# Optimization experiments

Measured on AMD Instinct MI355X. Metric: run time of the kernel, lower is better.

The kernel has to match this reference:

```python
import jax, jax.numpy as jnp
import numpy as np

H, D, RPE_DIM, LAYERS = 8, 64, 64, 3
GAMMA = 0.999  # fixed decay (use_decay=True, requires_grad=False)
EPS = 1e-8

def simple_rmsnorm(x):
    # SimpleRMSNorm: x / (||x||_2 * d^{-1/2} + eps), no learned scale
    rms = jnp.sqrt(jnp.sum(x * x, axis=-1, keepdims=True)) * (x.shape[-1] ** -0.5)
    return x / (rms + EPS)

def rpe_transform(idx, pos_proj_w, pos_proj_b, layer_ws, layer_bs, out_w, out_b):
    # idx: (n, 1) -> (H, n, D)
    x = idx @ pos_proj_w + pos_proj_b            # (n, RPE_DIM)
    for i in range(LAYERS):                       # residual=False -> sequential
        x = jax.nn.relu(simple_rmsnorm(x)) @ layer_ws[i] + layer_bs[i]
    x = jax.nn.relu(simple_rmsnorm(x)) @ out_w + out_b   # (n, H*D)
    n = x.shape[0]
    return x.reshape(n, H, D).transpose(1, 0, 2)  # (H, n, D)

def setup_inputs() -> dict:
    key = jax.random.key(0)
    ks = jax.random.split(key, 6)
    b, n = 8, 4096
    s = RPE_DIM ** -0.5
    return {
        "x": jax.random.normal(ks[0], (b, H, n, D), jnp.float32),
        "pos_proj_w": jax.random.normal(ks[1], (1, RPE_DIM), jnp.float32),
        "pos_proj_b": jnp.zeros((RPE_DIM,), jnp.float32),
        "layer_ws": jax.random.normal(ks[2], (LAYERS, RPE_DIM, RPE_DIM), jnp.float32) * s,
        "layer_bs": jnp.zeros((LAYERS, RPE_DIM), jnp.float32),
        "out_w": jax.random.normal(ks[3], (RPE_DIM, H * D), jnp.float32) * s,
        "out_b": jnp.zeros((H * D,), jnp.float32),
    }

def reference(x, pos_proj_w, pos_proj_b, layer_ws, layer_bs, out_w, out_b):
    b, h, n, d = x.shape
    _rpe = lambda idx: rpe_transform(idx, pos_proj_w, pos_proj_b, layer_ws, layer_bs, out_w, out_b)
    # relative-position kernel values (par_type=1: raw integer offsets)
    zero = _rpe(jnp.zeros((1, 1), x.dtype))                       # (H, 1, D)
    pos_idx = jnp.arange(1, n, dtype=x.dtype).reshape(n - 1, 1)   # 1..n-1
    pos = _rpe(pos_idx)                                           # (H, n-1, D)
    neg = _rpe(-pos_idx[::-1])                                    # -(n-1)..-1
    # fixed exponential decay gamma^|offset|
    coef = jnp.arange(1, n, dtype=x.dtype).reshape(1, n - 1, 1)
    gamma = jnp.full((h, 1, d), GAMMA, x.dtype) ** coef           # (H, n-1, D)
    pos = gamma * pos
    neg = gamma[:, ::-1, :] * neg
    # act_type='none' -> identity activation on a
    a = jnp.concatenate([zero, pos, zero, neg], axis=1)           # (H, 2n, D)
    # circular conv of length 2n realizes the Toeplitz matvec
    y = jnp.fft.rfft(x, n=2 * n, axis=-2)                         # (b,H,n+1?,D) complex
    v = jnp.fft.rfft(a, n=2 * n, axis=-2)[None]                   # (1,H,.,D)
    out = jnp.fft.irfft(v * y, n=2 * n, axis=-2)[:, :, :n, :]
    return out
```

## Files before the change

kernel.cpp:

```cpp
#include <hip/hip_runtime.h>
#include <math.h>

#define NF 8192

__device__ __forceinline__ int phys(int e) { return e ^ (((e >> 4) & 7) << 1); }

__device__ __forceinline__ float2 cmul(float2 a, float2 b) {
    return make_float2(a.x*b.x - a.y*b.y, a.x*b.y + a.y*b.x);
}
__device__ __forceinline__ float2 cmulc(float2 a, float2 b) {
    return make_float2(a.x*b.x + a.y*b.y, a.y*b.x - a.x*b.y);
}
__device__ __forceinline__ float2 cadd(float2 a, float2 b){ return make_float2(a.x+b.x, a.y+b.y); }
__device__ __forceinline__ float2 csub(float2 a, float2 b){ return make_float2(a.x-b.x, a.y-b.y); }
__device__ __forceinline__ float2 mnegi(float2 a){ return make_float2(a.y, -a.x); }
__device__ __forceinline__ float2 mposi(float2 a){ return make_float2(-a.y, a.x); }
#define RSQ2 0.70710678118654752f
__device__ __forceinline__ float2 mw81 (float2 a){ return make_float2( RSQ2*(a.x+a.y),  RSQ2*(a.y-a.x)); }
__device__ __forceinline__ float2 mw83 (float2 a){ return make_float2( RSQ2*(a.y-a.x), -RSQ2*(a.x+a.y)); }
__device__ __forceinline__ float2 mw81c(float2 a){ return make_float2( RSQ2*(a.x-a.y),  RSQ2*(a.x+a.y)); }
__device__ __forceinline__ float2 mw83c(float2 a){ return make_float2(-RSQ2*(a.x+a.y),  RSQ2*(a.x-a.y)); }

#define C16_1 0.92387953251128674f
#define S16_1 0.38268343236508978f
#define C16_2 0.70710678118654752f

__device__ __forceinline__ void dif8_core(float2& v0, float2& v1, float2& v2, float2& v3,
                                          float2& v4, float2& v5, float2& v6, float2& v7) {
    float2 t;
    t = csub(v0, v4); v0 = cadd(v0, v4); v4 = t;
    t = csub(v1, v5); v1 = cadd(v1, v5); v5 = mw81(t);
    t = csub(v2, v6); v2 = cadd(v2, v6); v6 = mnegi(t);
    t = csub(v3, v7); v3 = cadd(v3, v7); v7 = mw83(t);
    t = csub(v0, v2); v0 = cadd(v0, v2); v2 = t;
    t = csub(v1, v3); v1 = cadd(v1, v3); v3 = mnegi(t);
    t = csub(v4, v6); v4 = cadd(v4, v6); v6 = t;
    t = csub(v5, v7); v5 = cadd(v5, v7); v7 = mnegi(t);
    t = csub(v0, v1); v0 = cadd(v0, v1); v1 = t;
    t = csub(v2, v3); v2 = cadd(v2, v3); v3 = t;
    t = csub(v4, v5); v4 = cadd(v4, v5); v5 = t;
    t = csub(v6, v7); v6 = cadd(v6, v7); v7 = t;
}

__device__ __forceinline__ void dit8_core(float2& v0, float2& v1, float2& v2, float2& v3,
                                          float2& v4, float2& v5, float2& v6, float2& v7) {
    float2 t;
    t = csub(v0, v1); v0 = cadd(v0, v1); v1 = t;
    t = csub(v2, v3); v2 = cadd(v2, v3); v3 = t;
    t = csub(v4, v5); v4 = cadd(v4, v5); v5 = t;
    t = csub(v6, v7); v6 = cadd(v6, v7); v7 = t;
    t = v2;        v2 = csub(v0, t); v0 = cadd(v0, t);
    t = mposi(v3); v3 = csub(v1, t); v1 = cadd(v1, t);
    t = v6;        v6 = csub(v4, t); v4 = cadd(v4, t);
    t = mposi(v7); v7 = csub(v5, t); v5 = cadd(v5, t);
    t = v4;        v4 = csub(v0, t); v0 = cadd(v0, t);
    t = mw81c(v5); v5 = csub(v1, t); v1 = cadd(v1, t);
    t = mposi(v6); v6 = csub(v2, t); v2 = cadd(v2, t);
    t = mw83c(v7); v7 = csub(v3, t); v3 = cadd(v3, t);
}

template<int M, int LM>
__device__ __forceinline__ void fwd8_lds(float2* Z, const float2* __restrict__ tw, int tid) {
    #pragma unroll
    for (int q = 0; q < 2; ++q) {
        int beta = tid + q*512;
        int i    = beta & (M-1);
        int base = ((beta >> LM) << (LM+3)) + i;
        float2 v0 = Z[phys(base        )];
        float2 v1 = Z[phys(base + 1*M)];
        float2 v2 = Z[phys(base + 2*M)];
        float2 v3 = Z[phys(base + 3*M)];
        float2 v4 = Z[phys(base + 4*M)];
        float2 v5 = Z[phys(base + 5*M)];
        float2 v6 = Z[phys(base + 6*M)];
        float2 v7 = Z[phys(base + 7*M)];
        dif8_core(v0,v1,v2,v3,v4,v5,v6,v7);
        int ts = (NF >> (LM+3)) * i;
        Z[phys(base        )] = v0;
        Z[phys(base + 4*M)] = cmul(v1, tw[ts*4]);
        Z[phys(base + 2*M)] = cmul(v2, tw[ts*2]);
        Z[phys(base + 6*M)] = cmul(v3, tw[ts*6]);
        Z[phys(base + 1*M)] = cmul(v4, tw[ts  ]);
        Z[phys(base + 5*M)] = cmul(v5, tw[ts*5]);
        Z[phys(base + 3*M)] = cmul(v6, tw[ts*3]);
        Z[phys(base + 7*M)] = cmul(v7, tw[ts*7]);
    }
}

template<int M, int LM>
__device__ __forceinline__ void inv8_lds(float2* Z, const float2* __restrict__ tw, int tid) {
    #pragma unroll
    for (int q = 0; q < 2; ++q) {
        int beta = tid + q*512;
        int i    = beta & (M-1);
        int base = ((beta >> LM) << (LM+3)) + i;
        int ts   = (NF >> (LM+3)) * i;
        float2 v0 = Z[phys(base        )];
        float2 v1 = cmulc(Z[phys(base + 4*M)], tw[ts*4]);
        float2 v2 = cmulc(Z[phys(base + 2*M)], tw[ts*2]);
        float2 v3 = cmulc(Z[phys(base + 6*M)], tw[ts*6]);
        float2 v4 = cmulc(Z[phys(base + 1*M)], tw[ts  ]);
        float2 v5 = cmulc(Z[phys(base + 5*M)], tw[ts*5]);
        float2 v6 = cmulc(Z[phys(base + 3*M)], tw[ts*3]);
        float2 v7 = cmulc(Z[phys(base + 7*M)], tw[ts*7]);
        dit8_core(v0,v1,v2,v3,v4,v5,v6,v7);
        Z[phys(base        )] = v0;
        Z[phys(base + 1*M)] = v1;
        Z[phys(base + 2*M)] = v2;
        Z[phys(base + 3*M)] = v3;
        Z[phys(base + 4*M)] = v4;
        Z[phys(base + 5*M)] = v5;
        Z[phys(base + 6*M)] = v6;
        Z[phys(base + 7*M)] = v7;
    }
}

__global__ void twiddle_kernel(float2* __restrict__ tw) {
    int j = blockIdx.x * 256 + threadIdx.x;
    double ang = -6.283185307179586476925286766559 * (double)j / 8192.0;
    tw[j] = make_float2((float)cos(ang), (float)sin(ang));
}

__global__ __launch_bounds__(256) void rpe_kernel(
    const float* __restrict__ pw,  const float* __restrict__ pb,
    const float* __restrict__ lws, const float* __restrict__ lbs,
    const float* __restrict__ ow,  const float* __restrict__ ob,
    float* __restrict__ a_buf)
{
    __shared__ float sW[3][64][64];
    __shared__ float sB[3][64];
    __shared__ float sPW[64], sPB[64];
    __shared__ float sAct[4][64];
    int tid = threadIdx.x;
    for (int idx = tid; idx < 3*64*64; idx += 256) ((float*)sW)[idx] = lws[idx];
    if (tid < 3*64) ((float*)sB)[tid] = lbs[tid];
    if (tid < 64) { sPW[tid] = pw[tid]; sPB[tid] = pb[tid]; }
    __syncthreads();

    int wave = tid >> 6, lane = tid & 63;
    int e = blockIdx.x * 4 + wave;
    float p = (e == 4096) ? 0.f : ((e < 4096) ? (float)e : (float)(e - 8192));
    int m = (e < 4096) ? e : (8192 - e);
    if (e == 4096) m = 0;
    float dec = exp2f(-0.0014434309482562475f * (float)m);

    float xv = fmaf(p, sPW[lane], sPB[lane]);
    for (int L = 0; L < 3; ++L) {
        float ss = xv * xv;
        #pragma unroll
        for (int o = 1; o < 64; o <<= 1) ss += __shfl_xor(ss, o);
        float act = fmaxf(xv / (sqrtf(ss) * 0.125f + 1e-8f), 0.f);
        sAct[wave][lane] = act;
        __syncthreads();
        float y0 = sB[L][lane], y1 = 0.f;
        #pragma unroll
        for (int k = 0; k < 64; k += 2) {
            y0 = fmaf(sAct[wave][k],   sW[L][k][lane],   y0);
            y1 = fmaf(sAct[wave][k+1], sW[L][k+1][lane], y1);
        }
        __syncthreads();
        xv = y0 + y1;
    }
    {
        float ss = xv * xv;
        #pragma unroll
        for (int o = 1; o < 64; o <<= 1) ss += __shfl_xor(ss, o);
        sAct[wave][lane] = fmaxf(xv / (sqrtf(ss) * 0.125f + 1e-8f), 0.f);
    }
    auto& sWo = sW[0];
    float res[8];
    for (int qq = 0; qq < 8; ++qq) {
        __syncthreads();
        for (int idx = tid; idx < 4096; idx += 256)
            ((float*)sWo)[idx] = ow[(size_t)(idx >> 6)*512 + qq*64 + (idx & 63)];
        __syncthreads();
        float y0 = ob[qq*64 + lane], y1 = 0.f, y2 = 0.f, y3 = 0.f;
        #pragma unroll
        for (int k = 0; k < 64; k += 4) {
            y0 = fmaf(sAct[wave][k],   sWo[k  ][lane], y0);
            y1 = fmaf(sAct[wave][k+1], sWo[k+1][lane], y1);
            y2 = fmaf(sAct[wave][k+2], sWo[k+2][lane], y2);
            y3 = fmaf(sAct[wave][k+3], sWo[k+3][lane], y3);
        }
        res[qq] = (y0+y1+y2+y3) * dec;
    }
    #pragma unroll
    for (int qq = 0; qq < 8; ++qq)
        a_buf[(size_t)(qq*64 + lane)*NF + e] = res[qq];
}

__global__ __launch_bounds__(512, 4) void afft_kernel(
    const float* __restrict__ a_buf, const float2* __restrict__ tw,
    float2* __restrict__ Afft)
{
    __shared__ __align__(16) float2 Z[NF];
    int cc = blockIdx.x, tid = threadIdx.x;
    const float* col = a_buf + (size_t)cc * NF;
    #pragma unroll
    for (int q = 0; q < 2; ++q) {
        int i = tid + q*512;
        float2 v0 = make_float2(col[i       ], 0.f);
        float2 v1 = make_float2(col[i + 1024], 0.f);
        float2 v2 = make_float2(col[i + 2048], 0.f);
        float2 v3 = make_float2(col[i + 3072], 0.f);
        float2 v4 = make_float2(col[i + 4096], 0.f);
        float2 v5 = make_float2(col[i + 5120], 0.f);
        float2 v6 = make_float2(col[i + 6144], 0.f);
        float2 v7 = make_float2(col[i + 7168], 0.f);
        dif8_core(v0,v1,v2,v3,v4,v5,v6,v7);
        int ts = i;
        Z[phys(i        )] = v0;
        Z[phys(i + 4096)] = cmul(v1, tw[ts*4]);
        Z[phys(i + 2048)] = cmul(v2, tw[ts*2]);
        Z[phys(i + 6144)] = cmul(v3, tw[ts*6]);
        Z[phys(i + 1024)] = cmul(v4, tw[ts  ]);
        Z[phys(i + 5120)] = cmul(v5, tw[ts*5]);
        Z[phys(i + 3072)] = cmul(v6, tw[ts*3]);
        Z[phys(i + 7168)] = cmul(v7, tw[ts*7]);
    }
    __syncthreads();
    fwd8_lds<128, 7>(Z, tw, tid);  __syncthreads();
    fwd8_lds<16,  4>(Z, tw, tid);  __syncthreads();
    {
        int c = tid, sw4 = c & 7;
        float4* Z4 = reinterpret_cast<float4*>(Z);
        float4* oc4 = reinterpret_cast<float4*>(Afft + (size_t)cc * NF);
        float2 z[16];
        #pragma unroll
        for (int j = 0; j < 8; ++j) {
            float4 wv = Z4[c*8 + (j ^ sw4)];
            z[2*j]   = make_float2(wv.x, wv.y);
            z[2*j+1] = make_float2(wv.z, wv.w);
        }
        dif8_core(z[0],z[2],z[4],z[6],z[8],z[10],z[12],z[14]);
        dif8_core(z[1],z[3],z[5],z[7],z[9],z[11],z[13],z[15]);
        #define A4K(k, ZE, ZO, WR, WI) { \
            float2 w = make_float2((WR)*(ZO).x - (WI)*(ZO).y, (WR)*(ZO).y + (WI)*(ZO).x); \
            float2 pp = cadd(ZE, w), rr = csub(ZE, w); \
            oc4[c*8 + (k)] = make_float4(pp.x, pp.y, rr.x, rr.y); }
        { float2 pp = cadd(z[0], z[1]), rr = csub(z[0], z[1]);
          oc4[c*8 + 0] = make_float4(pp.x, pp.y, rr.x, rr.y); }
        A4K(1, z[8],  z[9],   C16_1, -S16_1)
        A4K(2, z[4],  z[5],   C16_2, -C16_2)
        A4K(3, z[12], z[13],  S16_1, -C16_1)
        { float2 w = mnegi(z[3]);
          float2 pp = cadd(z[2], w), rr = csub(z[2], w);
          oc4[c*8 + 4] = make_float4(pp.x, pp.y, rr.x, rr.y); }
        A4K(5, z[10], z[11], -S16_1, -C16_1)
        A4K(6, z[6],  z[7],  -C16_2, -C16_2)
        A4K(7, z[14], z[15], -C16_1, -S16_1)
        #undef A4K
    }
}

__global__ __launch_bounds__(512, 4) void conv_kernel(
    const float* __restrict__ x, const float2* __restrict__ tw,
    const float2* __restrict__ Afft, float* __restrict__ out)
{
    __shared__ __align__(16) float2 Z[NF];
    int blk = blockIdx.x;
    int c8 = blk & 7, r = blk >> 3;
    int d  = ((c8 & 1) << 5) | (r & 31);
    int h  = (((r >> 5) & 3) << 1) | ((c8 >> 1) & 1);
    int bp = (((r >> 7) & 1) << 1) | ((c8 >> 2) & 1);
    int tid = threadIdx.x;
    size_t base0 = ((size_t)((bp*2 + 0)*8 + h) * 4096) * 64 + d;
    size_t base1 = ((size_t)((bp*2 + 1)*8 + h) * 4096) * 64 + d;

    #pragma unroll
    for (int q = 0; q < 2; ++q) {
        int i = tid + q*512;
        float2 v0 = make_float2(x[base0 + (size_t)(i       )*64], x[base1 + (size_t)(i       )*64]);
        float2 v1 = make_float2(x[base0 + (size_t)(i + 1024)*64], x[base1 + (size_t)(i + 1024)*64]);
        float2 v2 = make_float2(x[base0 + (size_t)(i + 2048)*64], x[base1 + (size_t)(i + 2048)*64]);
        float2 v3 = make_float2(x[base0 + (size_t)(i + 3072)*64], x[base1 + (size_t)(i + 3072)*64]);
        float2 v4 = v0;
        float2 v5 = mw81(v1);
        float2 v6 = mnegi(v2);
        float2 v7 = mw83(v3);
        float2 t;
        t = csub(v0, v2); v0 = cadd(v0, v2); v2 = t;
        t = csub(v1, v3); v1 = cadd(v1, v3); v3 = mnegi(t);
        t = csub(v4, v6); v4 = cadd(v4, v6); v6 = t;
        t = csub(v5, v7); v5 = cadd(v5, v7); v7 = mnegi(t);
        t = csub(v0, v1); v0 = cadd(v0, v1); v1 = t;
        t = csub(v2, v3); v2 = cadd(v2, v3); v3 = t;
        t = csub(v4, v5); v4 = cadd(v4, v5); v5 = t;
        t = csub(v6, v7); v6 = cadd(v6, v7); v7 = t;
        int ts = i;
        Z[phys(i        )] = v0;
        Z[phys(i + 4096)] = cmul(v1, tw[ts*4]);
        Z[phys(i + 2048)] = cmul(v2, tw[ts*2]);
        Z[phys(i + 6144)] = cmul(v3, tw[ts*6]);
        Z[phys(i + 1024)] = cmul(v4, tw[ts  ]);
        Z[phys(i + 5120)] = cmul(v5, tw[ts*5]);
        Z[phys(i + 3072)] = cmul(v6, tw[ts*3]);
        Z[phys(i + 7168)] = cmul(v7, tw[ts*7]);
    }
    __syncthreads();
    fwd8_lds<128, 7>(Z, tw, tid);  __syncthreads();
    fwd8_lds<16,  4>(Z, tw, tid);  __syncthreads();

    {
        int c = tid, sw4 = c & 7;
        float4* Z4 = reinterpret_cast<float4*>(Z);
        const float4* A4 = reinterpret_cast<const float4*>(Afft + (size_t)(h*64 + d)*NF);
        float2 z[16];
        #pragma unroll
        for (int j = 0; j < 8; ++j) {
            float4 wv = Z4[c*8 + (j ^ sw4)];
            z[2*j]   = make_float2(wv.x, wv.y);
            z[2*j+1] = make_float2(wv.z, wv.w);
        }
        dif8_core(z[0],z[2],z[4],z[6],z[8],z[10],z[12],z[14]);
        dif8_core(z[1],z[3],z[5],z[7],z[9],z[11],z[13],z[15]);
        #define P4K(k, ZE, ZO, WR, WI) { \
            float2 w = make_float2((WR)*(ZO).x - (WI)*(ZO).y, (WR)*(ZO).y + (WI)*(ZO).x); \
            float2 pp = cadd(ZE, w), rr = csub(ZE, w); \
            float4 av = A4[c*8 + (k)]; \
            pp = cmul(pp, make_float2(av.x, av.y)); \
            rr = cmul(rr, make_float2(av.z, av.w)); \
            ZE = cadd(pp, rr); \
            ZO = csub(pp, rr); }
        { float2 pp = cadd(z[0], z[1]), rr = csub(z[0], z[1]);
          float4 av = A4[c*8 + 0];
          pp = cmul(pp, make_float2(av.x, av.y));
          rr = cmul(rr, make_float2(av.z, av.w));
          z[0] = cadd(pp, rr); z[1] = csub(pp, rr); }
        P4K(1, z[8],  z[9],   C16_1, -S16_1)
        P4K(2, z[4],  z[5],   C16_2, -C16_2)
        P4K(3, z[12], z[13],  S16_1, -C16_1)
        { float2 w = mnegi(z[3]);
          float2 pp = cadd(z[2], w), rr = csub(z[2], w);
          float4 av = A4[c*8 + 4];
          pp = cmul(pp, make_float2(av.x, av.y));
          rr = cmul(rr, make_float2(av.z, av.w));
          z[2] = cadd(pp, rr); z[3] = csub(pp, rr); }
        P4K(5, z[10], z[11], -S16_1, -C16_1)
        P4K(6, z[6],  z[7],  -C16_2, -C16_2)
        P4K(7, z[14], z[15], -C16_1, -S16_1)
        #undef P4K
        z[3]  = mposi(z[3]);
        z[5]  = cmul(z[5],  make_float2( C16_2,  C16_2));
        z[7]  = cmul(z[7],  make_float2(-C16_2,  C16_2));
        z[9]  = cmul(z[9],  make_float2( C16_1,  S16_1));
        z[11] = cmul(z[11], make_float2(-S16_1,  C16_1));
        z[13] = cmul(z[13], make_float2( S16_1,  C16_1));
        z[15] = cmul(z[15], make_float2(-C16_1,  S16_1));
        dit8_core(z[0],z[2],z[4],z[6],z[8],z[10],z[12],z[14]);
        dit8_core(z[1],z[3],z[5],z[7],z[9],z[11],z[13],z[15]);
        #pragma unroll
        for (int j = 0; j < 8; ++j)
            Z4[c*8 + (j ^ sw4)] = make_float4(z[2*j].x, z[2*j].y, z[2*j+1].x, z[2*j+1].y);
    }
    __syncthreads();
    inv8_lds<16,  4>(Z, tw, tid);  __syncthreads();
    inv8_lds<128, 7>(Z, tw, tid);  __syncthreads();

    const float sc = 1.0f/8192.0f;
    #pragma unroll
    for (int q = 0; q < 2; ++q) {
        int i = tid + q*512;
        int ts = i;
        float2 v0 = Z[phys(i        )];
        float2 v1 = cmulc(Z[phys(i + 4096)], tw[ts*4]);
        float2 v2 = cmulc(Z[phys(i + 2048)], tw[ts*2]);
        float2 v3 = cmulc(Z[phys(i + 6144)], tw[ts*6]);
        float2 v4 = cmulc(Z[phys(i + 1024)], tw[ts  ]);
        float2 v5 = cmulc(Z[phys(i + 5120)], tw[ts*5]);
        float2 v6 = cmulc(Z[phys(i + 3072)], tw[ts*3]);
        float2 v7 = cmulc(Z[phys(i + 7168)], tw[ts*7]);
        float2 t;
        t = csub(v0, v1); v0 = cadd(v0, v1); v1 = t;
        t = csub(v2, v3); v2 = cadd(v2, v3); v3 = t;
        t = csub(v4, v5); v4 = cadd(v4, v5); v5 = t;
        t = csub(v6, v7); v6 = cadd(v6, v7); v7 = t;
        t = v2;        v2 = csub(v0, t); v0 = cadd(v0, t);
        t = mposi(v3); v3 = csub(v1, t); v1 = cadd(v1, t);
        t = v6;        v6 = csub(v4, t); v4 = cadd(v4, t);
        t = mposi(v7); v7 = csub(v5, t); v5 = cadd(v5, t);
        v0 = cadd(v0, v4);
        v1 = cadd(v1, mw81c(v5));
        v2 = cadd(v2, mposi(v6));
        v3 = cadd(v3, mw83c(v7));
        out[base0 + (size_t)(i       )*64] = v0.x * sc;
        out[base1 + (size_t)(i       )*64] = v0.y * sc;
        out[base0 + (size_t)(i + 1024)*64] = v1.x * sc;
        out[base1 + (size_t)(i + 1024)*64] = v1.y * sc;
        out[base0 + (size_t)(i + 2048)*64] = v2.x * sc;
        out[base1 + (size_t)(i + 2048)*64] = v2.y * sc;
        out[base0 + (size_t)(i + 3072)*64] = v3.x * sc;
        out[base1 + (size_t)(i + 3072)*64] = v3.y * sc;
    }
}

extern "C" void kernel_launch(void* const* d_in, const int* in_sizes, int n_in,
                              void* d_out, int out_size, void* d_ws, size_t ws_size,
                              hipStream_t stream) {
    const float* x   = (const float*)d_in[0];
    const float* pw  = (const float*)d_in[1];
    const float* pb  = (const float*)d_in[2];
    const float* lws = (const float*)d_in[3];
    const float* lbs = (const float*)d_in[4];
    const float* ow  = (const float*)d_in[5];
    const float* ob  = (const float*)d_in[6];
    float* out = (float*)d_out;
    char* ws = (char*)d_ws;
    float2* tw    = (float2*)ws;
    float*  a_buf = (float*)(ws + 65536);
    float2* Afft  = (float2*)(ws + 65536 + (size_t)512*NF*4);

    twiddle_kernel<<<32, 256, 0, stream>>>(tw);
    rpe_kernel<<<2048, 256, 0, stream>>>(pw, pb, lws, lbs, ow, ob, a_buf);
    afft_kernel<<<512, 512, 0, stream>>>(a_buf, tw, Afft);
    conv_kernel<<<2048, 512, 0, stream>>>(x, tw, Afft, out);
}
```

Baseline: 586.5 us.

## Compute FFT twiddles on the fly, batch RPE MLP, and coalesce spectrum layout

Removes the twiddle table kernel and instead computes twiddles in registers from a hardware sin/cos of the base angle plus complex powers, avoiding global twiddle loads. The RPE MLP kernel now processes 4 positions per wave with 512 threads, cutting syncs and reusing the staged output weights across positions. The Afft layout is transposed to [k][c], so adjacent threads read adjacent float4 entries in the conv kernel. Risks include lower twiddle accuracy from native sin/cos and from chained power multiplication, and extra ALU work in the FFT stages.

```diff
diff --git a/kernel.cpp b/kernel.cpp
--- a/kernel.cpp
+++ b/kernel.cpp
@@ -24,6 +24,11 @@
 #define C16_1 0.92387953251128674f
 #define S16_1 0.38268343236508978f
 #define C16_2 0.70710678118654752f
+
+__device__ __forceinline__ float2 twbase(int ts) {
+    float fa = (float)ts * (1.0f/8192.0f);
+    return make_float2(__builtin_amdgcn_cosf(fa), -__builtin_amdgcn_sinf(fa));
+}
 
 __device__ __forceinline__ void dif8_core(float2& v0, float2& v1, float2& v2, float2& v3,
                                           float2& v4, float2& v5, float2& v6, float2& v7) {
@@ -59,8 +64,17 @@
     t = mw83c(v7); v7 = csub(v3, t); v3 = cadd(v3, t);
 }
 
+#define TW_POWERS(ts) \
+    float2 w1 = twbase(ts); \
+    float2 w2 = cmul(w1, w1); \
+    float2 w3 = cmul(w2, w1); \
+    float2 w4 = cmul(w2, w2); \
+    float2 w5 = cmul(w3, w2); \
+    float2 w6 = cmul(w3, w3); \
+    float2 w7 = cmul(w4, w3);
+
 template<int M, int LM>
-__device__ __forceinline__ void fwd8_lds(float2* Z, const float2* __restrict__ tw, int tid) {
+__device__ __forceinline__ void fwd8_lds(float2* Z, int tid) {
     #pragma unroll
     for (int q = 0; q < 2; ++q) {
         int beta = tid + q*512;
@@ -75,34 +89,34 @@
         float2 v6 = Z[phys(base + 6*M)];
         float2 v7 = Z[phys(base + 7*M)];
         dif8_core(v0,v1,v2,v3,v4,v5,v6,v7);
-        int ts = (NF >> (LM+3)) * i;
+        TW_POWERS((NF >> (LM+3)) * i)
         Z[phys(base        )] = v0;
-        Z[phys(base + 4*M)] = cmul(v1, tw[ts*4]);
-        Z[phys(base + 2*M)] = cmul(v2, tw[ts*2]);
-        Z[phys(base + 6*M)] = cmul(v3, tw[ts*6]);
-        Z[phys(base + 1*M)] = cmul(v4, tw[ts  ]);
-        Z[phys(base + 5*M)] = cmul(v5, tw[ts*5]);
-        Z[phys(base + 3*M)] = cmul(v6, tw[ts*3]);
-        Z[phys(base + 7*M)] = cmul(v7, tw[ts*7]);
+        Z[phys(base + 4*M)] = cmul(v1, w4);
+        Z[phys(base + 2*M)] = cmul(v2, w2);
+        Z[phys(base + 6*M)] = cmul(v3, w6);
+        Z[phys(base + 1*M)] = cmul(v4, w1);
+        Z[phys(base + 5*M)] = cmul(v5, w5);
+        Z[phys(base + 3*M)] = cmul(v6, w3);
+        Z[phys(base + 7*M)] = cmul(v7, w7);
     }
 }
 
 template<int M, int LM>
-__device__ __forceinline__ void inv8_lds(float2* Z, const float2* __restrict__ tw, int tid) {
+__device__ __forceinline__ void inv8_lds(float2* Z, int tid) {
     #pragma unroll
     for (int q = 0; q < 2; ++q) {
         int beta = tid + q*512;
         int i    = beta & (M-1);
         int base = ((beta >> LM) << (LM+3)) + i;
-        int ts   = (NF >> (LM+3)) * i;
+        TW_POWERS((NF >> (LM+3)) * i)
         float2 v0 = Z[phys(base        )];
-        float2 v1 = cmulc(Z[phys(base + 4*M)], tw[ts*4]);
-        float2 v2 = cmulc(Z[phys(base + 2*M)], tw[ts*2]);
-        float2 v3 = cmulc(Z[phys(base + 6*M)], tw[ts*6]);
-        float2 v4 = cmulc(Z[phys(base + 1*M)], tw[ts  ]);
-        float2 v5 = cmulc(Z[phys(base + 5*M)], tw[ts*5]);
-        float2 v6 = cmulc(Z[phys(base + 3*M)], tw[ts*3]);
-        float2 v7 = cmulc(Z[phys(base + 7*M)], tw[ts*7]);
+        float2 v1 = cmulc(Z[phys(base + 4*M)], w4);
+        float2 v2 = cmulc(Z[phys(base + 2*M)], w2);
+        float2 v3 = cmulc(Z[phys(base + 6*M)], w6);
+        float2 v4 = cmulc(Z[phys(base + 1*M)], w1);
+        float2 v5 = cmulc(Z[phys(base + 5*M)], w5);
+        float2 v6 = cmulc(Z[phys(base + 3*M)], w3);
+        float2 v7 = cmulc(Z[phys(base + 7*M)], w7);
         dit8_core(v0,v1,v2,v3,v4,v5,v6,v7);
         Z[phys(base        )] = v0;
         Z[phys(base + 1*M)] = v1;
@@ -115,83 +129,83 @@
     }
 }
 
-__global__ void twiddle_kernel(float2* __restrict__ tw) {
-    int j = blockIdx.x * 256 + threadIdx.x;
-    double ang = -6.283185307179586476925286766559 * (double)j / 8192.0;
-    tw[j] = make_float2((float)cos(ang), (float)sin(ang));
-}
-
-__global__ __launch_bounds__(256) void rpe_kernel(
+
+__global__ __launch_bounds__(512) void rpe_kernel(
     const float* __restrict__ pw,  const float* __restrict__ pb,
     const float* __restrict__ lws, const float* __restrict__ lbs,
     const float* __restrict__ ow,  const float* __restrict__ ob,
     float* __restrict__ a_buf)
 {
     __shared__ float sW[3][64][64];
+    __shared__ float sWo[64][64];
     __shared__ float sB[3][64];
     __shared__ float sPW[64], sPB[64];
-    __shared__ float sAct[4][64];
+    __shared__ float sAct[8][4][64];
     int tid = threadIdx.x;
-    for (int idx = tid; idx < 3*64*64; idx += 256) ((float*)sW)[idx] = lws[idx];
-    if (tid < 3*64) ((float*)sB)[tid] = lbs[tid];
+    for (int idx = tid; idx < 3*64*64; idx += 512) ((float*)sW)[idx] = lws[idx];
+    if (tid < 192) ((float*)sB)[tid] = lbs[tid];
     if (tid < 64) { sPW[tid] = pw[tid]; sPB[tid] = pb[tid]; }
     __syncthreads();
 
-    int wave = tid >> 6, lane = tid & 63;
-    int e = blockIdx.x * 4 + wave;
-    float p = (e == 4096) ? 0.f : ((e < 4096) ? (float)e : (float)(e - 8192));
-    int m = (e < 4096) ? e : (8192 - e);
-    if (e == 4096) m = 0;
-    float dec = exp2f(-0.0014434309482562475f * (float)m);
-
-    float xv = fmaf(p, sPW[lane], sPB[lane]);
-    for (int L = 0; L < 3; ++L) {
+    int wv = tid >> 6, lane = tid & 63;
+    int e0 = blockIdx.x * 32 + wv * 4;
+    float dec[4];
+    #pragma unroll
+    for (int s = 0; s < 4; ++s) {
+        int e = e0 + s;
+        float p = (e == 4096) ? 0.f : ((e < 4096) ? (float)e : (float)(e - 8192));
+        int m = (e < 4096) ? e : (8192 - e);
+        if (e == 4096) m = 0;
+        dec[s] = exp2f(-0.0014434309482562475f * (float)m);
+
+        float xv = fmaf(p, sPW[lane], sPB[lane]);
+        #pragma unroll
+        for (int L = 0; L < 3; ++L) {
+            float ss = xv * xv;
+            #pragma unroll
+            for (int o = 1; o < 64; o <<= 1) ss += __shfl_xor(ss, o);
+            sAct[wv][s][lane] = fmaxf(xv / (sqrtf(ss) * 0.125f + 1e-8f), 0.f);
+            float y = sB[L][lane];
+            const float4* av = reinterpret_cast<const float4*>(sAct[wv][s]);
+            #pragma unroll
+            for (int k = 0; k < 16; ++k) {
+                float4 a4 = av[k];
+                y = fmaf(a4.x, sW[L][4*k  ][lane], y);
+                y = fmaf(a4.y, sW[L][4*k+1][lane], y);
+                y = fmaf(a4.z, sW[L][4*k+2][lane], y);
+                y = fmaf(a4.w, sW[L][4*k+3][lane], y);
+            }
+            xv = y;
+        }
         float ss = xv * xv;
         #pragma unroll
         for (int o = 1; o < 64; o <<= 1) ss += __shfl_xor(ss, o);
-        float act = fmaxf(xv / (sqrtf(ss) * 0.125f + 1e-8f), 0.f);
-        sAct[wave][lane] = act;
-        __syncthreads();
-        float y0 = sB[L][lane], y1 = 0.f;
-        #pragma unroll
-        for (int k = 0; k < 64; k += 2) {
-            y0 = fmaf(sAct[wave][k],   sW[L][k][lane],   y0);
-            y1 = fmaf(sAct[wave][k+1], sW[L][k+1][lane], y1);
-        }
-        __syncthreads();
-        xv = y0 + y1;
-    }
-    {
-        float ss = xv * xv;
-        #pragma unroll
-        for (int o = 1; o < 64; o <<= 1) ss += __shfl_xor(ss, o);
-        sAct[wave][lane] = fmaxf(xv / (sqrtf(ss) * 0.125f + 1e-8f), 0.f);
-    }
-    auto& sWo = sW[0];
-    float res[8];
+        sAct[wv][s][lane] = fmaxf(xv / (sqrtf(ss) * 0.125f + 1e-8f), 0.f);
+    }
     for (int qq = 0; qq < 8; ++qq) {
         __syncthreads();
-        for (int idx = tid; idx < 4096; idx += 256)
+        for (int idx = tid; idx < 4096; idx += 512)
             ((float*)sWo)[idx] = ow[(size_t)(idx >> 6)*512 + qq*64 + (idx & 63)];
         __syncthreads();
-        float y0 = ob[qq*64 + lane], y1 = 0.f, y2 = 0.f, y3 = 0.f;
-        #pragma unroll
-        for (int k = 0; k < 64; k += 4) {
-            y0 = fmaf(sAct[wave][k],   sWo[k  ][lane], y0);
-            y1 = fmaf(sAct[wave][k+1], sWo[k+1][lane], y1);
-            y2 = fmaf(sAct[wave][k+2], sWo[k+2][lane], y2);
-            y3 = fmaf(sAct[wave][k+3], sWo[k+3][lane], y3);
+        #pragma unroll
+        for (int s = 0; s < 4; ++s) {
+            float y = ob[qq*64 + lane];
+            const float4* av = reinterpret_cast<const float4*>(sAct[wv][s]);
+            #pragma unroll
+            for (int k = 0; k < 16; ++k) {
+                float4 a4 = av[k];
+                y = fmaf(a4.x, sWo[4*k  ][lane], y);
+                y = fmaf(a4.y, sWo[4*k+1][lane], y);
+                y = fmaf(a4.z, sWo[4*k+2][lane], y);
+                y = fmaf(a4.w, sWo[4*k+3][lane], y);
+            }
+            a_buf[(size_t)(qq*64 + lane)*NF + (e0 + s)] = y * dec[s];
         }
-        res[qq] = (y0+y1+y2+y3) * dec;
-    }
-    #pragma unroll
-    for (int qq = 0; qq < 8; ++qq)
-        a_buf[(size_t)(qq*64 + lane)*NF + e] = res[qq];
+    }
 }
 
 __global__ __launch_bounds__(512, 4) void afft_kernel(
-    const float* __restrict__ a_buf, const float2* __restrict__ tw,
-    float2* __restrict__ Afft)
+    const float* __restrict__ a_buf, float2* __restrict__ Afft)
 {
     __shared__ __align__(16) float2 Z[NF];
     int cc = blockIdx.x, tid = threadIdx.x;
@@ -208,19 +222,19 @@
         float2 v6 = make_float2(col[i + 6144], 0.f);
         float2 v7 = make_float2(col[i + 7168], 0.f);
         dif8_core(v0,v1,v2,v3,v4,v5,v6,v7);
-        int ts = i;
+        TW_POWERS(i)
         Z[phys(i        )] = v0;
-        Z[phys(i + 4096)] = cmul(v1, tw[ts*4]);
-        Z[phys(i + 2048)] = cmul(v2, tw[ts*2]);
-        Z[phys(i + 6144)] = cmul(v3, tw[ts*6]);
-        Z[phys(i + 1024)] = cmul(v4, tw[ts  ]);
-        Z[phys(i + 5120)] = cmul(v5, tw[ts*5]);
-        Z[phys(i + 3072)] = cmul(v6, tw[ts*3]);
-        Z[phys(i + 7168)] = cmul(v7, tw[ts*7]);
+        Z[phys(i + 4096)] = cmul(v1, w4);
+        Z[phys(i + 2048)] = cmul(v2, w2);
+        Z[phys(i + 6144)] = cmul(v3, w6);
+        Z[phys(i + 1024)] = cmul(v4, w1);
+        Z[phys(i + 5120)] = cmul(v5, w5);
+        Z[phys(i + 3072)] = cmul(v6, w3);
+        Z[phys(i + 7168)] = cmul(v7, w7);
     }
     __syncthreads();
-    fwd8_lds<128, 7>(Z, tw, tid);  __syncthreads();
-    fwd8_lds<16,  4>(Z, tw, tid);  __syncthreads();
+    fwd8_lds<128, 7>(Z, tid);  __syncthreads();
+    fwd8_lds<16,  4>(Z, tid);  __syncthreads();
     {
         int c = tid, sw4 = c & 7;
         float4* Z4 = reinterpret_cast<float4*>(Z);
@@ -237,15 +251,15 @@
         #define A4K(k, ZE, ZO, WR, WI) { \
             float2 w = make_float2((WR)*(ZO).x - (WI)*(ZO).y, (WR)*(ZO).y + (WI)*(ZO).x); \
             float2 pp = cadd(ZE, w), rr = csub(ZE, w); \
-            oc4[c*8 + (k)] = make_float4(pp.x, pp.y, rr.x, rr.y); }
+            oc4[(k)*512 + c] = make_float4(pp.x, pp.y, rr.x, rr.y); }
         { float2 pp = cadd(z[0], z[1]), rr = csub(z[0], z[1]);
-          oc4[c*8 + 0] = make_float4(pp.x, pp.y, rr.x, rr.y); }
+          oc4[0*512 + c] = make_float4(pp.x, pp.y, rr.x, rr.y); }
         A4K(1, z[8],  z[9],   C16_1, -S16_1)
         A4K(2, z[4],  z[5],   C16_2, -C16_2)
         A4K(3, z[12], z[13],  S16_1, -C16_1)
         { float2 w = mnegi(z[3]);
           float2 pp = cadd(z[2], w), rr = csub(z[2], w);
-          oc4[c*8 + 4] = make_float4(pp.x, pp.y, rr.x, rr.y); }
+          oc4[4*512 + c] = make_float4(pp.x, pp.y, rr.x, rr.y); }
         A4K(5, z[10], z[11], -S16_1, -C16_1)
         A4K(6, z[6],  z[7],  -C16_2, -C16_2)
         A4K(7, z[14], z[15], -C16_1, -S16_1)
@@ -254,8 +268,8 @@
 }
 
 __global__ __launch_bounds__(512, 4) void conv_kernel(
-    const float* __restrict__ x, const float2* __restrict__ tw,
-    const float2* __restrict__ Afft, float* __restrict__ out)
+    const float* __restrict__ x, const float2* __restrict__ Afft,
+    float* __restrict__ out)
 {
     __shared__ __align__(16) float2 Z[NF];
     int blk = blockIdx.x;
@@ -287,19 +301,19 @@
         t = csub(v2, v3); v2 = cadd(v2, v3); v3 = t;
         t = csub(v4, v5); v4 = cadd(v4, v5); v5 = t;
         t = csub(v6, v7); v6 = cadd(v6, v7); v7 = t;
-        int ts = i;
+        TW_POWERS(i)
         Z[phys(i        )] = v0;
-        Z[phys(i + 4096)] = cmul(v1, tw[ts*4]);
-        Z[phys(i + 2048)] = cmul(v2, tw[ts*2]);
-        Z[phys(i + 6144)] = cmul(v3, tw[ts*6]);
-        Z[phys(i + 1024)] = cmul(v4, tw[ts  ]);
-        Z[phys(i + 5120)] = cmul(v5, tw[ts*5]);
-        Z[phys(i + 3072)] = cmul(v6, tw[ts*3]);
-        Z[phys(i + 7168)] = cmul(v7, tw[ts*7]);
+        Z[phys(i + 4096)] = cmul(v1, w4);
+        Z[phys(i + 2048)] = cmul(v2, w2);
+        Z[phys(i + 6144)] = cmul(v3, w6);
+        Z[phys(i + 1024)] = cmul(v4, w1);
+        Z[phys(i + 5120)] = cmul(v5, w5);
+        Z[phys(i + 3072)] = cmul(v6, w3);
+        Z[phys(i + 7168)] = cmul(v7, w7);
     }
     __syncthreads();
-    fwd8_lds<128, 7>(Z, tw, tid);  __syncthreads();
-    fwd8_lds<16,  4>(Z, tw, tid);  __syncthreads();
+    fwd8_lds<128, 7>(Z, tid);  __syncthreads();
+    fwd8_lds<16,  4>(Z, tid);  __syncthreads();
 
     {
         int c = tid, sw4 = c & 7;
@@ -317,13 +331,13 @@
         #define P4K(k, ZE, ZO, WR, WI) { \
             float2 w = make_float2((WR)*(ZO).x - (WI)*(ZO).y, (WR)*(ZO).y + (WI)*(ZO).x); \
             float2 pp = cadd(ZE, w), rr = csub(ZE, w); \
-            float4 av = A4[c*8 + (k)]; \
+            float4 av = A4[(k)*512 + c]; \
             pp = cmul(pp, make_float2(av.x, av.y)); \
             rr = cmul(rr, make_float2(av.z, av.w)); \
             ZE = cadd(pp, rr); \
             ZO = csub(pp, rr); }
         { float2 pp = cadd(z[0], z[1]), rr = csub(z[0], z[1]);
-          float4 av = A4[c*8 + 0];
+          float4 av = A4[0*512 + c];
           pp = cmul(pp, make_float2(av.x, av.y));
           rr = cmul(rr, make_float2(av.z, av.w));
           z[0] = cadd(pp, rr); z[1] = csub(pp, rr); }
@@ -332,7 +346,7 @@
         P4K(3, z[12], z[13],  S16_1, -C16_1)
         { float2 w = mnegi(z[3]);
           float2 pp = cadd(z[2], w), rr = csub(z[2], w);
-          float4 av = A4[c*8 + 4];
+          float4 av = A4[4*512 + c];
           pp = cmul(pp, make_float2(av.x, av.y));
           rr = cmul(rr, make_float2(av.z, av.w));
           z[2] = cadd(pp, rr); z[3] = csub(pp, rr); }
@@ -354,22 +368,22 @@
             Z4[c*8 + (j ^ sw4)] = make_float4(z[2*j].x, z[2*j].y, z[2*j+1].x, z[2*j+1].y);
     }
     __syncthreads();
-    inv8_lds<16,  4>(Z, tw, tid);  __syncthreads();
-    inv8_lds<128, 7>(Z, tw, tid);  __syncthreads();
+    inv8_lds<16,  4>(Z, tid);  __syncthreads();
+    inv8_lds<128, 7>(Z, tid);  __syncthreads();
 
     const float sc = 1.0f/8192.0f;
     #pragma unroll
     for (int q = 0; q < 2; ++q) {
         int i = tid + q*512;
-        int ts = i;
+        TW_POWERS(i)
         float2 v0 = Z[phys(i        )];
-        float2 v1 = cmulc(Z[phys(i + 4096)], tw[ts*4]);
-        float2 v2 = cmulc(Z[phys(i + 2048)], tw[ts*2]);
-        float2 v3 = cmulc(Z[phys(i + 6144)], tw[ts*6]);
-        float2 v4 = cmulc(Z[phys(i + 1024)], tw[ts  ]);
-        float2 v5 = cmulc(Z[phys(i + 5120)], tw[ts*5]);
-        float2 v6 = cmulc(Z[phys(i + 3072)], tw[ts*3]);
-        float2 v7 = cmulc(Z[phys(i + 7168)], tw[ts*7]);
+        float2 v1 = cmulc(Z[phys(i + 4096)], w4);
+        float2 v2 = cmulc(Z[phys(i + 2048)], w2);
+        float2 v3 = cmulc(Z[phys(i + 6144)], w6);
+        float2 v4 = cmulc(Z[phys(i + 1024)], w1);
+        float2 v5 = cmulc(Z[phys(i + 5120)], w5);
+        float2 v6 = cmulc(Z[phys(i + 3072)], w3);
+        float2 v7 = cmulc(Z[phys(i + 7168)], w7);
         float2 t;
         t = csub(v0, v1); v0 = cadd(v0, v1); v1 = t;
         t = csub(v2, v3); v2 = cadd(v2, v3); v3 = t;
@@ -406,12 +420,10 @@
     const float* ob  = (const float*)d_in[6];
     float* out = (float*)d_out;
     char* ws = (char*)d_ws;
-    float2* tw    = (float2*)ws;
-    float*  a_buf = (float*)(ws + 65536);
-    float2* Afft  = (float2*)(ws + 65536 + (size_t)512*NF*4);
-
-    twiddle_kernel<<<32, 256, 0, stream>>>(tw);
-    rpe_kernel<<<2048, 256, 0, stream>>>(pw, pb, lws, lbs, ow, ob, a_buf);
-    afft_kernel<<<512, 512, 0, stream>>>(a_buf, tw, Afft);
-    conv_kernel<<<2048, 512, 0, stream>>>(x, tw, Afft, out);
-}
+    float*  a_buf = (float*)ws;
+    float2* Afft  = (float2*)(ws + (size_t)512*NF*4);
+
+    rpe_kernel<<<256, 512, 0, stream>>>(pw, pb, lws, lbs, ow, ob, a_buf);
+    afft_kernel<<<512, 512, 0, stream>>>(a_buf, Afft);
+    conv_kernel<<<2048, 512, 0, stream>>>(x, Afft, out);
+}
```

Result: faster. 543.2 us (-7.4%).
